# Performance work log

Hardware: AMD Instinct MI355X
Metric: run time of the kernel (lower is better)

The kernel has to match this reference:

```python
import jax, jax.numpy as jnp
import numpy as np

VOCAB = 4096
CODE_DIM = 3


def setup_inputs() -> dict:
    key = jax.random.key(0)
    k1, k2 = jax.random.split(key)
    B, L = 4, 16384
    feats = jax.random.normal(k1, (B, L, CODE_DIM), dtype=jnp.float32)
    # xavier_uniform init for the (vocab, code_dim) embedding table
    limit = float(np.sqrt(6.0 / (VOCAB + CODE_DIM)))
    codebook = jax.random.uniform(k2, (VOCAB, CODE_DIM), dtype=jnp.float32,
                                  minval=-limit, maxval=limit)
    return {"feats": feats, "codebook": codebook}


def reference(feats, codebook):
    """EMAVQ.forward (eval mode): cdist -> argmin -> gather -> vq loss -> straight-through."""
    B, L, D = feats.shape
    flat = feats.reshape(-1, D)                      # (N, D)
    dist = (jnp.sum(flat * flat, axis=1, keepdims=True)
            - 2.0 * (flat @ codebook.T)
            + jnp.sum(codebook * codebook, axis=1))  # (N, V)
    idx = jnp.argmin(dist, axis=1)                   # (N,)
    quant = codebook[idx].reshape(B, L, D)           # embedding gather
    sg = jax.lax.stop_gradient
    loss = (jnp.mean((quant - sg(feats)) ** 2)
            + 0.25 * jnp.mean((feats - sg(quant)) ** 2))
    quant_st = feats + sg(quant - feats)             # straight-through estimator
    return quant_st, idx.reshape(B, L), loss
```

## Files before the change

### kernel.cpp

```cpp
#include <hip/hip_runtime.h>

#define VOCAB 4096
#define SLICES 16
#define SLICE 256
#define GRP 8
#define NGRP (SLICE / GRP)
#define P 4
#define PTS (64 * P)
#define THREADS 1024

__device__ __forceinline__ float opaque(float x) {
  asm volatile("" : "+v"(x));
  return x;
}

__device__ __forceinline__ float max3f(float a, float b, float c) {
  float d;
  asm("v_max3_f32 %0, %1, %2, %3" : "=v"(d) : "v"(a), "v"(b), "v"(c));
  return d;
}

__global__ __launch_bounds__(256) void vq_prep_kernel(
    const float* __restrict__ cb, float4* __restrict__ cw,
    float* __restrict__ loss_slot) {
  int j = blockIdx.x * 256 + threadIdx.x;
  if (j == 0) *loss_slot = 0.0f;
  if (j < VOCAB) {
    float e0 = cb[3 * j + 0];
    float e1 = cb[3 * j + 1];
    float e2 = cb[3 * j + 2];
    float p0 = opaque(e0 * e0);
    float p1 = opaque(e1 * e1);
    float p2 = opaque(e2 * e2);
    float c = opaque(opaque(p0 + p1) + p2);
    cw[j] = make_float4(e0, e1, e2, -0.5f * c);
  }
}

__device__ __forceinline__ float tval(float x0, float x1, float x2,
                                      float4 cd) {
  return fmaf(x0, cd.x, fmaf(x1, cd.y, fmaf(x2, cd.z, cd.w)));
}

__device__ __forceinline__ float dist_f32(float x0, float x1, float x2,
                                          float a, float4 cd) {
  float m = fmaf(x2, cd.z, fmaf(x1, cd.y, x0 * cd.x));
  return fmaf(-2.0f, m, a) + (-2.0f * cd.w);
}

__global__ __launch_bounds__(THREADS) void vq_kernel(
    const float* __restrict__ feats, const float4* __restrict__ cw,
    float* __restrict__ out_quant, float* __restrict__ out_idx,
    float* __restrict__ out_loss, int npts) {
  __shared__ float4 sTab[VOCAB];
  __shared__ float sT1[SLICES * PTS];
  __shared__ float sT2[SLICES * PTS];
  __shared__ int sG[SLICES * PTS];
  __shared__ unsigned long long sSlot[PTS];
  __shared__ int sList[PTS];
  __shared__ int sCount;
  __shared__ double sL[PTS];

  const int tid = threadIdx.x;
  const int lane = tid & 63;
  const int s = tid >> 6;

  if (tid == 0) sCount = 0;

#pragma unroll
  for (int k = 0; k < VOCAB / THREADS; ++k)
    sTab[tid + k * THREADS] = cw[tid + k * THREADS];

  const int pbase = blockIdx.x * PTS;
  float px[P], py[P], pz[P], nn[P];
#pragma unroll
  for (int k = 0; k < P; ++k) {
    const int p = pbase + k * 64 + lane;
    px[k] = feats[3 * p + 0];
    py[k] = feats[3 * p + 1];
    pz[k] = feats[3 * p + 2];
    float q0 = opaque(px[k] * px[k]);
    float q1 = opaque(py[k] * py[k]);
    float q2 = opaque(pz[k] * pz[k]);
    nn[k] = opaque(opaque(q0 + q1) + q2);
  }

  __syncthreads();

  const float4* cs = sTab + s * SLICE;

  float t1[P], t2[P];
  int gg[P];
#pragma unroll
  for (int k = 0; k < P; ++k) { t1[k] = -3.4e38f; t2[k] = -3.4e38f; gg[k] = 0; }
#pragma unroll 2
  for (int g = 0; g < NGRP; ++g) {
    const float4* gp = cs + g * GRP;
    float4 c0 = gp[0], c1 = gp[1], c2 = gp[2], c3 = gp[3];
    float4 c4 = gp[4], c5 = gp[5], c6 = gp[6], c7 = gp[7];
#pragma unroll
    for (int k = 0; k < P; ++k) {
      float u0 = tval(px[k], py[k], pz[k], c0);
      float u1 = tval(px[k], py[k], pz[k], c1);
      float u2 = tval(px[k], py[k], pz[k], c2);
      float u3 = tval(px[k], py[k], pz[k], c3);
      float u4 = tval(px[k], py[k], pz[k], c4);
      float u5 = tval(px[k], py[k], pz[k], c5);
      float u6 = tval(px[k], py[k], pz[k], c6);
      float u7 = tval(px[k], py[k], pz[k], c7);
      float gm = max3f(max3f(u0, u1, u2), max3f(u3, u4, u5), fmaxf(u6, u7));
      t2[k] = fmaxf(t2[k], fminf(t1[k], gm));
      if (gm > t1[k]) gg[k] = g;
      t1[k] = fmaxf(t1[k], gm);
    }
  }
#pragma unroll
  for (int k = 0; k < P; ++k) {
    sT1[s * PTS + k * 64 + lane] = t1[k];
    sT2[s * PTS + k * 64 + lane] = t2[k];
    sG[s * PTS + k * 64 + lane] = s * SLICE + gg[k] * GRP;
  }
  __syncthreads();

  int bi = 0;
  float q0 = 0.0f, q1 = 0.0f, q2 = 0.0f;
  bool flagged = false;
  float x0 = px[0], x1 = py[0], x2 = pz[0], a = nn[0];
#pragma unroll
  for (int k = 1; k < P; ++k) {
    if (s == k) { x0 = px[k]; x1 = py[k]; x2 = pz[k]; a = nn[k]; }
  }
  if (tid < PTS) {
    float b1 = sT1[tid], b2 = sT2[tid];
    int gbase = sG[tid];
#pragma unroll
    for (int k = 1; k < SLICES; ++k) {
      float u1 = sT1[k * PTS + tid];
      float u2 = sT2[k * PTS + tid];
      b2 = fmaxf(fmaxf(b2, u2), fminf(b1, u1));
      if (u1 > b1) gbase = sG[k * PTS + tid];
      b1 = fmaxf(b1, u1);
    }
    float eps = fmaf(a, 0x1p-21f, 0x1p-20f);
    flagged = !((b1 - b2) > eps);
    if (flagged) {
      int pos = atomicAdd(&sCount, 1);
      sList[pos] = tid;
      sSlot[tid] = ~0ULL;
    } else {
      float bd = 3.4e38f;
#pragma unroll
      for (int k = 0; k < GRP; ++k) {
        float4 cd = sTab[gbase + k];
        float d = dist_f32(x0, x1, x2, a, cd);
        if (d < bd) { bd = d; bi = gbase + k; q0 = cd.x; q1 = cd.y; q2 = cd.z; }
      }
    }
  }
  __syncthreads();

  const int cnt = sCount;
  for (int f = 0; f < cnt; ++f) {
    const int fpt = sList[f];
    const int fp = pbase + fpt;
    float y0 = feats[3 * fp + 0];
    float y1 = feats[3 * fp + 1];
    float y2 = feats[3 * fp + 2];
    float yp0 = opaque(y0 * y0);
    float yp1 = opaque(y1 * y1);
    float yp2 = opaque(y2 * y2);
    float ay = opaque(opaque(yp0 + yp1) + yp2);
    float bd = 3.4e38f;
    int bj = 0;
#pragma unroll
    for (int k = 0; k < VOCAB / THREADS; ++k) {
      int j = tid + k * THREADS;
      float4 cd = sTab[j];
      float d = dist_f32(y0, y1, y2, ay, cd);
      if (d < bd) { bd = d; bj = j; }
    }
    unsigned b = __float_as_uint(bd);
    b = (b & 0x80000000u) ? ~b : (b | 0x80000000u);
    unsigned long long key = ((unsigned long long)b << 32) | (unsigned)bj;
#pragma unroll
    for (int off = 1; off < 64; off <<= 1) {
      unsigned long long o = __shfl_xor(key, off);
      key = (o < key) ? o : key;
    }
    if (lane == 0) atomicMin(&sSlot[fpt], key);
  }
  __syncthreads();

  if (tid < PTS) {
    if (flagged) {
      bi = (int)(unsigned)(sSlot[tid] & 0xFFFFFFFFu);
      float4 cd = sTab[bi];
      q0 = cd.x; q1 = cd.y; q2 = cd.z;
    }
    const int p = pbase + tid;
    float t0 = q0 - x0, t1d = q1 - x1, t2d = q2 - x2;
    out_quant[3 * p + 0] = x0 + t0;
    out_quant[3 * p + 1] = x1 + t1d;
    out_quant[3 * p + 2] = x2 + t2d;
    out_idx[p] = (float)bi;
    sL[tid] = (double)t0 * t0 + (double)t1d * t1d + (double)t2d * t2d;
  }
  __syncthreads();

  if (tid == 0) {
    double acc = 0.0;
#pragma unroll 8
    for (int k = 0; k < PTS; ++k) acc += sL[k];
    atomicAdd(out_loss, (float)(acc * (1.25 / ((double)npts * 3.0))));
  }
}

extern "C" void kernel_launch(void* const* d_in, const int* in_sizes, int n_in,
                              void* d_out, int out_size, void* d_ws,
                              size_t ws_size, hipStream_t stream) {
  const float* feats = (const float*)d_in[0];
  const float* cb = (const float*)d_in[1];
  const int npts = in_sizes[0] / 3;

  float* out = (float*)d_out;
  float* out_quant = out;
  float* out_idx = out + in_sizes[0];
  float* out_loss = out + in_sizes[0] + npts;

  float4* cw = (float4*)d_ws;

  vq_prep_kernel<<<VOCAB / 256, 256, 0, stream>>>(cb, cw, out_loss);
  vq_kernel<<<npts / PTS, THREADS, 0, stream>>>(feats, cw, out_quant, out_idx,
                                                out_loss, npts);
}
```

Measured before the change: 88.01 us.

## Interleave codebook pairs and use packed FP32 FMA for distance scoring

The prep kernel now writes the codebook in an interleaved layout where each pair of float4s holds two codes, so the main scan can score two codes per v_pk_fma_f32 instruction. This is meant to halve the VALU instruction count in the hot distance loop. The second-best tracking is also folded into a single v_med3_f32. The refinement, fallback and gather paths are rewritten to decode the interleaved layout, which adds some index arithmetic and selects.

```diff
diff --git a/kernel.cpp b/kernel.cpp
--- a/kernel.cpp
+++ b/kernel.cpp
@@ -9,9 +9,17 @@
 #define PTS (64 * P)
 #define THREADS 1024
 
+typedef float v2f __attribute__((ext_vector_type(2)));
+
 __device__ __forceinline__ float opaque(float x) {
   asm volatile("" : "+v"(x));
   return x;
+}
+
+__device__ __forceinline__ v2f pk_fma(v2f a, v2f b, v2f c) {
+  v2f d;
+  asm("v_pk_fma_f32 %0, %1, %2, %3" : "=v"(d) : "v"(a), "v"(b), "v"(c));
+  return d;
 }
 
 __device__ __forceinline__ float max3f(float a, float b, float c) {
@@ -19,33 +27,35 @@
   asm("v_max3_f32 %0, %1, %2, %3" : "=v"(d) : "v"(a), "v"(b), "v"(c));
   return d;
 }
+__device__ __forceinline__ float med3f(float a, float b, float c) {
+  float d;
+  asm("v_med3_f32 %0, %1, %2, %3" : "=v"(d) : "v"(a), "v"(b), "v"(c));
+  return d;
+}
 
 __global__ __launch_bounds__(256) void vq_prep_kernel(
     const float* __restrict__ cb, float4* __restrict__ cw,
     float* __restrict__ loss_slot) {
-  int j = blockIdx.x * 256 + threadIdx.x;
-  if (j == 0) *loss_slot = 0.0f;
-  if (j < VOCAB) {
-    float e0 = cb[3 * j + 0];
-    float e1 = cb[3 * j + 1];
-    float e2 = cb[3 * j + 2];
-    float p0 = opaque(e0 * e0);
-    float p1 = opaque(e1 * e1);
-    float p2 = opaque(e2 * e2);
-    float c = opaque(opaque(p0 + p1) + p2);
-    cw[j] = make_float4(e0, e1, e2, -0.5f * c);
-  }
-}
-
-__device__ __forceinline__ float tval(float x0, float x1, float x2,
-                                      float4 cd) {
-  return fmaf(x0, cd.x, fmaf(x1, cd.y, fmaf(x2, cd.z, cd.w)));
-}
-
-__device__ __forceinline__ float dist_f32(float x0, float x1, float x2,
-                                          float a, float4 cd) {
-  float m = fmaf(x2, cd.z, fmaf(x1, cd.y, x0 * cd.x));
-  return fmaf(-2.0f, m, a) + (-2.0f * cd.w);
+  int r = blockIdx.x * 256 + threadIdx.x;
+  if (r == 0) *loss_slot = 0.0f;
+  if (r >= VOCAB / 2) return;
+  int g = r >> 2, i = r & 3;
+  int a = g * 8 + i, b = a + 4;
+  float a0 = cb[3 * a + 0], a1 = cb[3 * a + 1], a2 = cb[3 * a + 2];
+  float b0 = cb[3 * b + 0], b1 = cb[3 * b + 1], b2 = cb[3 * b + 2];
+  float pa0 = opaque(a0 * a0), pa1 = opaque(a1 * a1), pa2 = opaque(a2 * a2);
+  float ha = -0.5f * opaque(opaque(pa0 + pa1) + pa2);
+  float pb0 = opaque(b0 * b0), pb1 = opaque(b1 * b1), pb2 = opaque(b2 * b2);
+  float hb = -0.5f * opaque(opaque(pb0 + pb1) + pb2);
+  cw[(size_t)(g * 8 + 2 * i)] = make_float4(a0, b0, a1, b1);
+  cw[(size_t)(g * 8 + 2 * i + 1)] = make_float4(a2, b2, ha, hb);
+}
+
+__device__ __forceinline__ float dist_f32s(float x0, float x1, float x2,
+                                           float a, float e0, float e1,
+                                           float e2, float h) {
+  float m = fmaf(x2, e2, fmaf(x1, e1, x0 * e0));
+  return fmaf(-2.0f, m, a) + (-2.0f * h);
 }
 
 __global__ __launch_bounds__(THREADS) void vq_kernel(
@@ -73,6 +83,7 @@
 
   const int pbase = blockIdx.x * PTS;
   float px[P], py[P], pz[P], nn[P];
+  v2f xx0[P], xx1[P], xx2[P];
 #pragma unroll
   for (int k = 0; k < P; ++k) {
     const int p = pbase + k * 64 + lane;
@@ -83,6 +94,9 @@
     float q1 = opaque(py[k] * py[k]);
     float q2 = opaque(pz[k] * pz[k]);
     nn[k] = opaque(opaque(q0 + q1) + q2);
+    xx0[k] = (v2f){px[k], px[k]};
+    xx1[k] = (v2f){py[k], py[k]};
+    xx2[k] = (v2f){pz[k], pz[k]};
   }
 
   __syncthreads();
@@ -96,20 +110,25 @@
 #pragma unroll 2
   for (int g = 0; g < NGRP; ++g) {
     const float4* gp = cs + g * GRP;
-    float4 c0 = gp[0], c1 = gp[1], c2 = gp[2], c3 = gp[3];
-    float4 c4 = gp[4], c5 = gp[5], c6 = gp[6], c7 = gp[7];
+    float4 F0 = gp[0], F1 = gp[1], F2 = gp[2], F3 = gp[3];
+    float4 F4 = gp[4], F5 = gp[5], F6 = gp[6], F7 = gp[7];
 #pragma unroll
     for (int k = 0; k < P; ++k) {
-      float u0 = tval(px[k], py[k], pz[k], c0);
-      float u1 = tval(px[k], py[k], pz[k], c1);
-      float u2 = tval(px[k], py[k], pz[k], c2);
-      float u3 = tval(px[k], py[k], pz[k], c3);
-      float u4 = tval(px[k], py[k], pz[k], c4);
-      float u5 = tval(px[k], py[k], pz[k], c5);
-      float u6 = tval(px[k], py[k], pz[k], c6);
-      float u7 = tval(px[k], py[k], pz[k], c7);
-      float gm = max3f(max3f(u0, u1, u2), max3f(u3, u4, u5), fmaxf(u6, u7));
-      t2[k] = fmaxf(t2[k], fminf(t1[k], gm));
+      v2f u0 = pk_fma(xx0[k], (v2f){F0.x, F0.y},
+               pk_fma(xx1[k], (v2f){F0.z, F0.w},
+               pk_fma(xx2[k], (v2f){F1.x, F1.y}, (v2f){F1.z, F1.w})));
+      v2f u1 = pk_fma(xx0[k], (v2f){F2.x, F2.y},
+               pk_fma(xx1[k], (v2f){F2.z, F2.w},
+               pk_fma(xx2[k], (v2f){F3.x, F3.y}, (v2f){F3.z, F3.w})));
+      v2f u2 = pk_fma(xx0[k], (v2f){F4.x, F4.y},
+               pk_fma(xx1[k], (v2f){F4.z, F4.w},
+               pk_fma(xx2[k], (v2f){F5.x, F5.y}, (v2f){F5.z, F5.w})));
+      v2f u3 = pk_fma(xx0[k], (v2f){F6.x, F6.y},
+               pk_fma(xx1[k], (v2f){F6.z, F6.w},
+               pk_fma(xx2[k], (v2f){F7.x, F7.y}, (v2f){F7.z, F7.w})));
+      float gm = max3f(max3f(u0.x, u0.y, u1.x), max3f(u1.y, u2.x, u2.y),
+                       fmaxf(u3.x, u3.y));
+      t2[k] = med3f(t2[k], t1[k], gm);
       if (gm > t1[k]) gg[k] = g;
       t1[k] = fmaxf(t1[k], gm);
     }
@@ -151,9 +170,14 @@
       float bd = 3.4e38f;
 #pragma unroll
       for (int k = 0; k < GRP; ++k) {
-        float4 cd = sTab[gbase + k];
-        float d = dist_f32(x0, x1, x2, a, cd);
-        if (d < bd) { bd = d; bi = gbase + k; q0 = cd.x; q1 = cd.y; q2 = cd.z; }
+        int i = k & 3;
+        bool hi = k >= 4;
+        float4 A = sTab[gbase + 2 * i];
+        float4 B = sTab[gbase + 2 * i + 1];
+        float e0 = hi ? A.y : A.x, e1 = hi ? A.w : A.z;
+        float e2 = hi ? B.y : B.x, h = hi ? B.w : B.z;
+        float d = dist_f32s(x0, x1, x2, a, e0, e1, e2, h);
+        if (d < bd) { bd = d; bi = gbase + k; q0 = e0; q1 = e1; q2 = e2; }
       }
     }
   }
@@ -174,9 +198,14 @@
     int bj = 0;
 #pragma unroll
     for (int k = 0; k < VOCAB / THREADS; ++k) {
-      int j = tid + k * THREADS;
-      float4 cd = sTab[j];
-      float d = dist_f32(y0, y1, y2, ay, cd);
+      int j = tid * (VOCAB / THREADS) + k;
+      int g8 = (j >> 3) << 3, i = j & 3;
+      bool hi = (j & 4) != 0;
+      float4 A = sTab[g8 + 2 * i];
+      float4 B = sTab[g8 + 2 * i + 1];
+      float e0 = hi ? A.y : A.x, e1 = hi ? A.w : A.z;
+      float e2 = hi ? B.y : B.x, h = hi ? B.w : B.z;
+      float d = dist_f32s(y0, y1, y2, ay, e0, e1, e2, h);
       if (d < bd) { bd = d; bj = j; }
     }
     unsigned b = __float_as_uint(bd);
@@ -194,8 +223,11 @@
   if (tid < PTS) {
     if (flagged) {
       bi = (int)(unsigned)(sSlot[tid] & 0xFFFFFFFFu);
-      float4 cd = sTab[bi];
-      q0 = cd.x; q1 = cd.y; q2 = cd.z;
+      int g8 = (bi >> 3) << 3, i = bi & 3;
+      bool hi = (bi & 4) != 0;
+      float4 A = sTab[g8 + 2 * i];
+      float4 B = sTab[g8 + 2 * i + 1];
+      q0 = hi ? A.y : A.x; q1 = hi ? A.w : A.z; q2 = hi ? B.y : B.x;
     }
     const int p = pbase + tid;
     float t0 = q0 - x0, t1d = q1 - x1, t2d = q2 - x2;
@@ -229,7 +261,8 @@
 
   float4* cw = (float4*)d_ws;
 
-  vq_prep_kernel<<<VOCAB / 256, 256, 0, stream>>>(cb, cw, out_loss);
+  vq_prep_kernel<<<(VOCAB / 2 + 255) / 256, 256, 0, stream>>>(cb, cw,
+                                                              out_loss);
   vq_kernel<<<npts / PTS, THREADS, 0, stream>>>(feats, cw, out_quant, out_idx,
                                                 out_loss, npts);
 }
```

After: 93.72 us. +6.5%, slower.

## Split codebook slice across wave halves with 8 points per lane

Applied to the files above, without the earlier changes.

Each wave now divides its 256-code slice into two 128-code halves, one per 32-lane half. Each lane handles 8 points instead of 4, so every codebook float4 read from LDS is reused across twice as many points. The two halves' top-2 results are merged with cross-lane shuffles before being written to shared memory. The top-2 update also uses v_med3 in place of a max/min pair. The cost is more registers per thread (8 points each with top-2 state), which may raise register pressure with 1024-thread blocks.

```diff
diff --git a/kernel.cpp b/kernel.cpp
--- a/kernel.cpp
+++ b/kernel.cpp
@@ -3,10 +3,11 @@
 #define VOCAB 4096
 #define SLICES 16
 #define SLICE 256
+#define HALFSLICE 128
 #define GRP 8
-#define NGRP (SLICE / GRP)
-#define P 4
-#define PTS (64 * P)
+#define NGRPH (HALFSLICE / GRP)
+#define P 8
+#define PTS 256
 #define THREADS 1024
 
 __device__ __forceinline__ float opaque(float x) {
@@ -17,6 +18,11 @@
 __device__ __forceinline__ float max3f(float a, float b, float c) {
   float d;
   asm("v_max3_f32 %0, %1, %2, %3" : "=v"(d) : "v"(a), "v"(b), "v"(c));
+  return d;
+}
+__device__ __forceinline__ float med3f(float a, float b, float c) {
+  float d;
+  asm("v_med3_f32 %0, %1, %2, %3" : "=v"(d) : "v"(a), "v"(b), "v"(c));
   return d;
 }
 
@@ -64,6 +70,8 @@
   const int tid = threadIdx.x;
   const int lane = tid & 63;
   const int s = tid >> 6;
+  const int m = lane & 31;
+  const int half = lane >> 5;
 
   if (tid == 0) sCount = 0;
 
@@ -75,7 +83,7 @@
   float px[P], py[P], pz[P], nn[P];
 #pragma unroll
   for (int k = 0; k < P; ++k) {
-    const int p = pbase + k * 64 + lane;
+    const int p = pbase + k * 32 + m;
     px[k] = feats[3 * p + 0];
     py[k] = feats[3 * p + 1];
     pz[k] = feats[3 * p + 2];
@@ -87,15 +95,16 @@
 
   __syncthreads();
 
-  const float4* cs = sTab + s * SLICE;
+  const int cbase = s * SLICE + half * HALFSLICE;
+  const float4* ch = sTab + cbase;
 
   float t1[P], t2[P];
   int gg[P];
 #pragma unroll
   for (int k = 0; k < P; ++k) { t1[k] = -3.4e38f; t2[k] = -3.4e38f; gg[k] = 0; }
 #pragma unroll 2
-  for (int g = 0; g < NGRP; ++g) {
-    const float4* gp = cs + g * GRP;
+  for (int g = 0; g < NGRPH; ++g) {
+    const float4* gp = ch + g * GRP;
     float4 c0 = gp[0], c1 = gp[1], c2 = gp[2], c3 = gp[3];
     float4 c4 = gp[4], c5 = gp[5], c6 = gp[6], c7 = gp[7];
 #pragma unroll
@@ -109,26 +118,37 @@
       float u6 = tval(px[k], py[k], pz[k], c6);
       float u7 = tval(px[k], py[k], pz[k], c7);
       float gm = max3f(max3f(u0, u1, u2), max3f(u3, u4, u5), fmaxf(u6, u7));
-      t2[k] = fmaxf(t2[k], fminf(t1[k], gm));
+      t2[k] = med3f(t2[k], t1[k], gm);
       if (gm > t1[k]) gg[k] = g;
       t1[k] = fmaxf(t1[k], gm);
     }
   }
 #pragma unroll
   for (int k = 0; k < P; ++k) {
-    sT1[s * PTS + k * 64 + lane] = t1[k];
-    sT2[s * PTS + k * 64 + lane] = t2[k];
-    sG[s * PTS + k * 64 + lane] = s * SLICE + gg[k] * GRP;
+    int gb = cbase + gg[k] * GRP;
+    float o1 = __shfl_xor(t1[k], 32);
+    float o2 = __shfl_xor(t2[k], 32);
+    int ob = __shfl_xor(gb, 32);
+    float tmin = fminf(t1[k], o1);
+    float m2 = fmaxf(fmaxf(t2[k], o2), tmin);
+    int mb = (o1 > t1[k]) ? ob : gb;
+    float m1 = fmaxf(t1[k], o1);
+    if (half == 0) {
+      sT1[s * PTS + k * 32 + m] = m1;
+      sT2[s * PTS + k * 32 + m] = m2;
+      sG[s * PTS + k * 32 + m] = mb;
+    }
   }
   __syncthreads();
 
   int bi = 0;
   float q0 = 0.0f, q1 = 0.0f, q2 = 0.0f;
   bool flagged = false;
+  const int ksel = tid >> 5;
   float x0 = px[0], x1 = py[0], x2 = pz[0], a = nn[0];
 #pragma unroll
   for (int k = 1; k < P; ++k) {
-    if (s == k) { x0 = px[k]; x1 = py[k]; x2 = pz[k]; a = nn[k]; }
+    if (ksel == k) { x0 = px[k]; x1 = py[k]; x2 = pz[k]; a = nn[k]; }
   }
   if (tid < PTS) {
     float b1 = sT1[tid], b2 = sT2[tid];
```

Result: no change. 88.78 us (+0.9%).
